# Kernel tuning notes

Hardware: AMD Instinct MI355X
Metric: run time of the kernel (lower is better)

Reference implementation:

```python
import jax, jax.numpy as jnp
import numpy as np

B, T, D, SD, CHUNK = 4, 4096, 1024, 512, 32


def setup_inputs() -> dict:
    key = jax.random.key(0)
    ks = jax.random.split(key, 6)
    sc_in = 1.0 / np.sqrt(D)
    sc_out = 1.0 / np.sqrt(2 * SD)
    return {
        "x": jax.random.normal(ks[0], (B, T, D), jnp.float32),
        "Wt": jax.random.normal(ks[1], (D, SD), jnp.float32) * sc_in,
        "bt": jnp.zeros((SD,), jnp.float32),
        "Wr": jax.random.normal(ks[2], (D, SD), jnp.float32) * sc_in,
        "br": jnp.zeros((SD,), jnp.float32),
        "Wi": jax.random.normal(ks[3], (D, 2 * SD), jnp.float32) * sc_in,
        "bi": jnp.zeros((2 * SD,), jnp.float32),
        "Wo": jax.random.normal(ks[4], (2 * SD, D), jnp.float32) * sc_out,
        "bo": jnp.zeros((D,), jnp.float32),
        "gamma": jnp.ones((D,), jnp.float32),
        "beta": jnp.zeros((D,), jnp.float32),
    }


def _rotation_scan(theta, retain, b_r, b_i, chunk):
    # theta/retain/b_*: [B, T, d]. Chunked linear recurrence h[t]=a[t]*h[t-1]+b[t]
    # with a[t] = retain[t]*e^{i theta[t]}, done in log-magnitude/angle space.
    Bsz, Tlen, d = theta.shape
    K = min(chunk, Tlen)
    n = Tlen // K  # T assumed divisible by K (4096 / 32)
    resh = lambda a: a.reshape(Bsz, n, K, d).transpose(1, 0, 2, 3)  # [n,B,K,d]
    th_c, rt_c, br_c, bi_c = resh(theta), resh(retain), resh(b_r), resh(b_i)

    def step(carry, xs):
        h_r, h_i = carry  # [B, d]
        th, rt, cb_r, cb_i = xs  # [B, K, d]
        cum_log_mag = jnp.cumsum(jnp.log(jnp.clip(rt, 1e-6, None)), axis=1)
        cum_mag = jnp.exp(cum_log_mag)
        cum_th = jnp.cumsum(th, axis=1)
        cum_cos = jnp.cos(cum_th)
        cum_sin = jnp.sin(cum_th)
        cum_a_r = cum_mag * cum_cos
        cum_a_i = cum_mag * cum_sin
        inv_mag = 1.0 / jnp.clip(cum_mag, 1e-8, None)
        inv_r = inv_mag * cum_cos          # cos(-t) = cos(t)
        inv_i = -inv_mag * cum_sin         # sin(-t) = -sin(t)
        scaled_b_r = inv_r * cb_r - inv_i * cb_i
        scaled_b_i = inv_r * cb_i + inv_i * cb_r
        cum_b_r = jnp.cumsum(scaled_b_r, axis=1)
        cum_b_i = jnp.cumsum(scaled_b_i, axis=1)
        tot_r = h_r[:, None] + cum_b_r
        tot_i = h_i[:, None] + cum_b_i
        ch_r = cum_a_r * tot_r - cum_a_i * tot_i
        ch_i = cum_a_r * tot_i + cum_a_i * tot_r
        return (ch_r[:, -1], ch_i[:, -1]), (ch_r, ch_i)

    h0 = (jnp.zeros((Bsz, d), theta.dtype), jnp.zeros((Bsz, d), theta.dtype))
    _, (out_r, out_i) = jax.lax.scan(step, h0, (th_c, rt_c, br_c, bi_c))
    back = lambda a: a.transpose(1, 0, 2, 3).reshape(Bsz, Tlen, d)
    return back(out_r), back(out_i)


def reference(x, Wt, bt, Wr, br, Wi, bi, Wo, bo, gamma, beta):
    d = Wt.shape[1]
    theta = x @ Wt + bt                       # [B,T,d]
    retain = jax.nn.sigmoid(x @ Wr + br)      # [B,T,d]
    inp = x @ Wi + bi                          # [B,T,2d]
    inp_r, inp_i = inp[..., :d], inp[..., d:]
    drive = 1.0 - retain
    out_r, out_i = _rotation_scan(theta, retain, drive * inp_r, drive * inp_i, CHUNK)
    out = jnp.concatenate([out_r, out_i], axis=-1)  # [B,T,2d]
    y = x + out @ Wo + bo
    mu = jnp.mean(y, axis=-1, keepdims=True)
    var = jnp.var(y, axis=-1, keepdims=True)
    return (y - mu) / jnp.sqrt(var + 1e-5) * gamma + beta
```

## Files before the change

kernel.cpp:

```cpp
#include <hip/hip_runtime.h>
#include <cstdint>


typedef __bf16 bf16x8 __attribute__((ext_vector_type(8)));
typedef float  f32x4  __attribute__((ext_vector_type(4)));
typedef ushort u16x8  __attribute__((ext_vector_type(8)));

#define AS1 __attribute__((address_space(1)))
#define AS3 __attribute__((address_space(3)))

__device__ __forceinline__ void gload16(const void* g, void* l) {
  __builtin_amdgcn_global_load_lds((const AS1 void*)g, (AS3 void*)l, 16, 0, 0);
}

__device__ __forceinline__ ushort f2bf(float f) {
  union { float f; uint32_t u; } v; v.f = f;
  uint32_t u = v.u;
  uint32_t r = u + 0x7FFFu + ((u >> 16) & 1u);
  return (ushort)(r >> 16);
}
__device__ __forceinline__ float bf2f(ushort u) {
  union { uint32_t x; float f; } v; v.x = (uint32_t)u << 16; return v.f;
}

__global__ __launch_bounds__(256) void tconv(const float* __restrict__ src, int R, int C,
                                             ushort* __restrict__ dst, int row_off) {
  __shared__ float tile[32][33];
  int tx = threadIdx.x, ty = threadIdx.y;
  int rb = blockIdx.y * 32, cb = blockIdx.x * 32;
#pragma unroll
  for (int yy = 0; yy < 4; ++yy) {
    int r = rb + ty + yy * 8;
    tile[ty + yy * 8][tx] = src[(size_t)r * C + cb + tx];
  }
  __syncthreads();
#pragma unroll
  for (int yy = 0; yy < 4; ++yy) {
    int c = cb + ty + yy * 8;
    dst[(size_t)(row_off + c) * R + rb + tx] = f2bf(tile[tx][ty + yy * 8]);
  }
}

__global__ __launch_bounds__(256) void pack_bias(const float* __restrict__ bt,
                                                 const float* __restrict__ br,
                                                 const float* __restrict__ bi,
                                                 float* __restrict__ bcat) {
  int i = blockIdx.x * 256 + threadIdx.x;
  bcat[i] = (i < 512) ? bt[i] : (i < 1024 ? br[i - 512] : bi[i - 1024]);
}

__global__ __launch_bounds__(256) void xconv(const float4* __restrict__ src,
                                             ushort* __restrict__ dst, int n4) {
  int i = blockIdx.x * 256 + threadIdx.x;
  if (i < n4) {
    float4 v = src[i];
    ushort4 o;
    o.x = f2bf(v.x); o.y = f2bf(v.y); o.z = f2bf(v.z); o.w = f2bf(v.w);
    *(ushort4*)(dst + (size_t)i * 4) = o;
  }
}

template <int BM>
__global__ __launch_bounds__(512, 2) void gemm256(const ushort* __restrict__ A,
                                                  const ushort* __restrict__ Bt,
                                                  ushort* __restrict__ C,
                                                  const float* __restrict__ bias,
                                                  int M, int N, int K, int nbn) {
  constexpr int MI = BM / 32;
  constexpr int II = BM / 128;
  constexpr int STAGE_USH = 2 * (BM * 64 + 256 * 64);
  constexpr int CT_USH = BM * 256;
  constexpr int SM_USH = (STAGE_USH > CT_USH) ? STAGE_USH : CT_USH;
  __shared__ alignas(16) ushort smem[SM_USH];
  ushort* const As0 = smem;
  ushort* const Bs0 = smem + 2 * BM * 64;

  const int cpx = gridDim.x >> 3;
  const int wg = ((int)blockIdx.x & 7) * cpx + ((int)blockIdx.x >> 3);
  const int bm = wg / nbn, bn = wg % nbn;

  const int t = threadIdx.x;
  const int l = t & 63, w = t >> 6;
  const int wm = w >> 2, wn = w & 3;
  const int r = l & 15, kq = l >> 4;

  const size_t a0 = (size_t)bm * BM * K;
  const size_t b0 = (size_t)bn * 256 * K;

  const int srow = t >> 3;
  const int sslot = (t & 7) ^ (srow & 7);
  const ushort* gA = A + a0 + (size_t)srow * K + sslot * 8;
  const ushort* gB = Bt + b0 + (size_t)srow * K + sslot * 8;
  const int lboff = w * 1024 + l * 16;

  f32x4 acc[MI][4] = {};
  const int NKT = K >> 6;

#define STGA(buf, kt, u) \
  gload16(gA + (size_t)((u) * 64) * K + (size_t)(kt) * 64, \
          (char*)(As0 + (buf) * BM * 64) + (u) * 8192 + lboff)
#define STGB(buf, kt, u) \
  gload16(gB + (size_t)((u) * 64) * K + (size_t)(kt) * 64, \
          (char*)(Bs0 + (buf) * 256 * 64) + (u) * 8192 + lboff)

#define QUAD(ph)                                                               \
  do {                                                                         \
    _Pragma("unroll")                                                          \
    for (int ii = 0; ii < II; ++ii) {                                          \
      bf16x8 aF[2];                                                            \
      const int rowa = wm * (BM / 2) + ((ph) * II + ii) * 16 + r;              \
      _Pragma("unroll")                                                        \
      for (int ks = 0; ks < 2; ++ks) {                                         \
        const int j = (ks * 4 + kq) ^ (r & 7);                                 \
        aF[ks] = *(const bf16x8*)&pA[rowa * 64 + j * 8];                       \
      }                                                                        \
      __builtin_amdgcn_s_setprio(1);                                           \
      _Pragma("unroll")                                                        \
      for (int jn = 0; jn < 4; ++jn)                                           \
        _Pragma("unroll")                                                      \
        for (int ks = 0; ks < 2; ++ks)                                         \
          acc[(ph) * II + ii][jn] = __builtin_amdgcn_mfma_f32_16x16x32_bf16(   \
              aF[ks], bF[jn][ks], acc[(ph) * II + ii][jn], 0, 0, 0);           \
      __builtin_amdgcn_s_setprio(0);                                           \
    }                                                                          \
  } while (0)

  STGB(0, 0, 0); STGB(0, 0, 1); STGB(0, 0, 2); STGB(0, 0, 3);
  if constexpr (BM == 256) { STGA(0, 0, 0); STGA(0, 0, 2); STGA(0, 0, 1); STGA(0, 0, 3); }
  else                     { STGA(0, 0, 0); STGA(0, 0, 1); }

  for (int kt = 0; kt < NKT; ++kt) {
    const int cur = kt & 1, nxt = cur ^ 1;
    const bool hn = (kt + 1 < NKT);
    const ushort* pA = As0 + cur * BM * 64;
    const ushort* pB = Bs0 + cur * 256 * 64;
    if (hn) { STGB(nxt, kt + 1, 0); STGB(nxt, kt + 1, 1); }
    if constexpr (BM == 256) {
      if (hn) asm volatile("s_waitcnt vmcnt(4)" ::: "memory");
      else    asm volatile("s_waitcnt vmcnt(2)" ::: "memory");
    } else {
      if (hn) asm volatile("s_waitcnt vmcnt(2)" ::: "memory");
      else    asm volatile("s_waitcnt vmcnt(0)" ::: "memory");
    }
    __builtin_amdgcn_s_barrier();
    asm volatile("" ::: "memory");
    bf16x8 bF[4][2];
#pragma unroll
    for (int jn = 0; jn < 4; ++jn) {
      const int rowb = wn * 64 + jn * 16 + r;
#pragma unroll
      for (int ks = 0; ks < 2; ++ks) {
        const int j = (ks * 4 + kq) ^ (r & 7);
        bF[jn][ks] = *(const bf16x8*)&pB[rowb * 64 + j * 8];
      }
    }
    QUAD(0);
    if (hn) { STGB(nxt, kt + 1, 2); STGB(nxt, kt + 1, 3); }
    QUAD(1);
    if (hn) {
      if constexpr (BM == 256) { STGA(nxt, kt + 1, 0); STGA(nxt, kt + 1, 2); }
      else                     { STGA(nxt, kt + 1, 0); }
    }
    if constexpr (BM == 256) {
      if (hn) asm volatile("s_waitcnt vmcnt(6)" ::: "memory");
      else    asm volatile("s_waitcnt vmcnt(0)" ::: "memory");
    }
    __builtin_amdgcn_s_barrier();
    asm volatile("" ::: "memory");
    QUAD(2);
    if (hn) {
      if constexpr (BM == 256) { STGA(nxt, kt + 1, 1); STGA(nxt, kt + 1, 3); }
      else                     { STGA(nxt, kt + 1, 1); }
    }
    QUAD(3);
  }
#undef STGA
#undef STGB
#undef QUAD

  asm volatile("s_waitcnt lgkmcnt(0) vmcnt(0)" ::: "memory");
  __builtin_amdgcn_s_barrier();

  const int q4 = (l >> 4) * 4;
  float bvj[4];
#pragma unroll
  for (int jn = 0; jn < 4; ++jn) {
    const int col = wn * 64 + jn * 16 + r;
    bvj[jn] = bias ? bias[bn * 256 + col] : 0.f;
  }
#pragma unroll
  for (int i = 0; i < MI; ++i) {
#pragma unroll
    for (int jn = 0; jn < 4; ++jn) {
      const int col = wn * 64 + jn * 16 + r;
      const int chunk = col >> 3;
#pragma unroll
      for (int q = 0; q < 4; ++q) {
        const int rowl = wm * (BM / 2) + i * 16 + q4 + q;
        const int pch = chunk ^ (rowl & 7);
        smem[rowl * 256 + pch * 8 + (col & 7)] = f2bf(acc[i][jn][q] + bvj[jn]);
      }
    }
  }
  __builtin_amdgcn_s_barrier();

  const int rrow0 = t >> 5;
  const int rch = t & 31;
#pragma unroll
  for (int p = 0; p < BM / 16; ++p) {
    const int rowl = p * 16 + rrow0;
    const int pch = rch ^ (rowl & 7);
    u16x8 vv = *(const u16x8*)&smem[rowl * 256 + pch * 8];
    const size_t grow = (size_t)(bm * BM + rowl);
    *(u16x8*)&C[grow * N + bn * 256 + rch * 8] = vv;
  }
}

__global__ __launch_bounds__(256) void scan_k1(const ushort* __restrict__ lin,
                                               float4* __restrict__ agg) {
  int bd = blockIdx.x * 256 + threadIdx.x;
  int c  = blockIdx.y;
  int b  = bd >> 9, d = bd & 511;
  const ushort* base = lin + ((size_t)b * 4096 + (size_t)c * 32) * 2048;
  float cth = 0.f, cbr = 0.f, cbi = 0.f;
  float cm = 1.f, cs = 1.f, sn = 0.f;
#pragma unroll 4
  for (int t = 0; t < 32; ++t) {
    const ushort* row = base + (size_t)t * 2048;
    float th = bf2f(row[d]);
    float z  = bf2f(row[512 + d]);
    float ir = bf2f(row[1024 + d]);
    float ii = bf2f(row[1536 + d]);
    float rt = __fdividef(1.f, 1.f + __expf(-z));
    cm *= fmaxf(rt, 1e-6f);
    cth += th;
    float s_, c_;
    __sincosf(cth, &s_, &c_);
    float im = __fdividef(1.f, fmaxf(cm, 1e-8f));
    float invr = im * c_, invi = -im * s_;
    float drive = 1.f - rt;
    float br_ = drive * ir, bi_ = drive * ii;
    cbr += invr * br_ - invi * bi_;
    cbi += invr * bi_ + invi * br_;
    cs = c_; sn = s_;
  }
  agg[(size_t)c * 2048 + bd] = make_float4(cm * cs, cm * sn, cbr, cbi);
}

__global__ __launch_bounds__(256) void scan_k2(const float4* __restrict__ agg,
                                               float2* __restrict__ h0) {
  int bd = blockIdx.x * 256 + threadIdx.x;
  float hr = 0.f, hi = 0.f;
  for (int cg = 0; cg < 16; ++cg) {
    float4 a[8];
#pragma unroll
    for (int u = 0; u < 8; ++u) a[u] = agg[(size_t)(cg * 8 + u) * 2048 + bd];
#pragma unroll
    for (int u = 0; u < 8; ++u) {
      h0[(size_t)(cg * 8 + u) * 2048 + bd] = make_float2(hr, hi);
      float tr = hr + a[u].z, ti = hi + a[u].w;
      hr = a[u].x * tr - a[u].y * ti;
      hi = a[u].x * ti + a[u].y * tr;
    }
  }
}

__global__ __launch_bounds__(256) void scan_k3(const ushort* __restrict__ lin,
                                               const float2* __restrict__ h0,
                                               ushort* __restrict__ outb) {
  int bd = blockIdx.x * 256 + threadIdx.x;
  int c  = blockIdx.y;
  int b  = bd >> 9, d = bd & 511;
  const ushort* base = lin + ((size_t)b * 4096 + (size_t)c * 32) * 2048;
  float2 h = h0[(size_t)c * 2048 + bd];
  float cth = 0.f, cbr = 0.f, cbi = 0.f, cm = 1.f;
#pragma unroll 4
  for (int t = 0; t < 32; ++t) {
    const ushort* row = base + (size_t)t * 2048;
    float th = bf2f(row[d]);
    float z  = bf2f(row[512 + d]);
    float ir = bf2f(row[1024 + d]);
    float ii = bf2f(row[1536 + d]);
    float rt = __fdividef(1.f, 1.f + __expf(-z));
    cm *= fmaxf(rt, 1e-6f);
    cth += th;
    float s_, c_;
    __sincosf(cth, &s_, &c_);
    float im = __fdividef(1.f, fmaxf(cm, 1e-8f));
    float invr = im * c_, invi = -im * s_;
    float drive = 1.f - rt;
    float br_ = drive * ir, bi_ = drive * ii;
    cbr += invr * br_ - invi * bi_;
    cbi += invr * bi_ + invi * br_;
    float ar = cm * c_, ai = cm * s_;
    float tr = h.x + cbr, ti = h.y + cbi;
    float orr = ar * tr - ai * ti;
    float oii = ar * ti + ai * tr;
    size_t rowo = ((size_t)b * 4096 + (size_t)c * 32 + t) * 1024;
    outb[rowo + d] = f2bf(orr);
    outb[rowo + 512 + d] = f2bf(oii);
  }
}

__global__ __launch_bounds__(256) void ln_k(const ushort* __restrict__ yb,
                                            const ushort* __restrict__ xb,
                                            const float* __restrict__ gamma,
                                            const float* __restrict__ beta,
                                            float* __restrict__ out) {
  int row = blockIdx.x;
  ushort4 uy = ((const ushort4*)(yb + (size_t)row * 1024))[threadIdx.x];
  ushort4 ux = ((const ushort4*)(xb + (size_t)row * 1024))[threadIdx.x];
  float4 v;
  v.x = bf2f(uy.x) + bf2f(ux.x);
  v.y = bf2f(uy.y) + bf2f(ux.y);
  v.z = bf2f(uy.z) + bf2f(ux.z);
  v.w = bf2f(uy.w) + bf2f(ux.w);
  float s  = v.x + v.y + v.z + v.w;
  float s2 = v.x * v.x + v.y * v.y + v.z * v.z + v.w * v.w;
#pragma unroll
  for (int off = 32; off > 0; off >>= 1) {
    s  += __shfl_down(s, off);
    s2 += __shfl_down(s2, off);
  }
  __shared__ float red[8];
  __shared__ float mv[2];
  int l = threadIdx.x & 63, w = threadIdx.x >> 6;
  if (l == 0) { red[w] = s; red[4 + w] = s2; }
  __syncthreads();
  if (threadIdx.x == 0) {
    float ts = red[0] + red[1] + red[2] + red[3];
    float t2 = red[4] + red[5] + red[6] + red[7];
    float mu = ts * (1.f / 1024.f);
    float var = t2 * (1.f / 1024.f) - mu * mu;
    mv[0] = mu;
    mv[1] = 1.f / sqrtf(var + 1e-5f);
  }
  __syncthreads();
  float mu = mv[0], rstd = mv[1];
  const float4* g4 = (const float4*)gamma;
  const float4* b4 = (const float4*)beta;
  float4 gv = g4[threadIdx.x], bv = b4[threadIdx.x];
  float4 o;
  o.x = (v.x - mu) * rstd * gv.x + bv.x;
  o.y = (v.y - mu) * rstd * gv.y + bv.y;
  o.z = (v.z - mu) * rstd * gv.z + bv.z;
  o.w = (v.w - mu) * rstd * gv.w + bv.w;
  ((float4*)(out + (size_t)row * 1024))[threadIdx.x] = o;
}

extern "C" void kernel_launch(void* const* d_in, const int* in_sizes, int n_in,
                              void* d_out, int out_size, void* d_ws, size_t ws_size,
                              hipStream_t stream) {
  (void)in_sizes; (void)n_in; (void)out_size; (void)ws_size;
  const float* x  = (const float*)d_in[0];
  const float* Wt = (const float*)d_in[1];
  const float* bt = (const float*)d_in[2];
  const float* Wr = (const float*)d_in[3];
  const float* br = (const float*)d_in[4];
  const float* Wi = (const float*)d_in[5];
  const float* bi = (const float*)d_in[6];
  const float* Wo = (const float*)d_in[7];
  const float* bo = (const float*)d_in[8];
  const float* gamma = (const float*)d_in[9];
  const float* beta  = (const float*)d_in[10];

  char* ws = (char*)d_ws;
  ushort* wcat_t = (ushort*)(ws);
  ushort* wo_t   = (ushort*)(ws + ((size_t)4  << 20));
  float*  bcat   = (float*) (ws + ((size_t)6  << 20));
  float4* agg    = (float4*)(ws + ((size_t)8  << 20));
  float2* h0     = (float2*)(ws + ((size_t)12 << 20));
  ushort* xb     = (ushort*)(ws + ((size_t)16 << 20));
  ushort* outb   = (ushort*)(ws + ((size_t)48 << 20));
  ushort* linb   = (ushort*)(ws + ((size_t)80 << 20));
  ushort* yb     = (ushort*)(ws + ((size_t)80 << 20));

  tconv<<<dim3(512 / 32, 1024 / 32), dim3(32, 8), 0, stream>>>(Wt, 1024, 512, wcat_t, 0);
  tconv<<<dim3(512 / 32, 1024 / 32), dim3(32, 8), 0, stream>>>(Wr, 1024, 512, wcat_t, 512);
  tconv<<<dim3(1024 / 32, 1024 / 32), dim3(32, 8), 0, stream>>>(Wi, 1024, 1024, wcat_t, 1024);
  tconv<<<dim3(1024 / 32, 1024 / 32), dim3(32, 8), 0, stream>>>(Wo, 1024, 1024, wo_t, 0);
  pack_bias<<<8, 256, 0, stream>>>(bt, br, bi, bcat);
  xconv<<<16384, 256, 0, stream>>>((const float4*)x, xb, 4194304);

  gemm256<256><<<512, 512, 0, stream>>>(xb, wcat_t, linb, bcat, 16384, 2048, 1024, 8);

  scan_k1<<<dim3(8, 128), 256, 0, stream>>>(linb, agg);
  scan_k2<<<8, 256, 0, stream>>>(agg, h0);
  scan_k3<<<dim3(8, 128), 256, 0, stream>>>(linb, h0, outb);

  gemm256<128><<<512, 512, 0, stream>>>(outb, wo_t, yb, bo, 16384, 1024, 1024, 4);

  ln_k<<<16384, 256, 0, stream>>>(yb, xb, gamma, beta, (float*)d_out);
}
```

Baseline: 213.3 us.

## Restructure GEMM mainloop into 4 barrier-separated phases with B prefetched two tiles ahead

Reorganizes the bf16 MFMA GEMM main loop into four phases, each loading its A fragments from LDS, issuing a slice of global-to-LDS staging, then running MFMAs between barriers. The B tile is now prefetched two k-steps ahead into the current buffer once it has been consumed, while A is prefetched one step ahead. The aim is to deepen the load pipeline and interleave LDS reads, global loads and MFMAs more evenly. In exchange it adds two barriers per phase (eight per k-step) and more fragment registers, and it depends on the hand-tuned vmcnt counts being correct.

Measured after the change: 217.4 us. About the same (+1.9%).

```diff
diff --git a/kernel.cpp b/kernel.cpp
--- a/kernel.cpp
+++ b/kernel.cpp
@@ -103,80 +103,98 @@
   gload16(gB + (size_t)((u) * 64) * K + (size_t)(kt) * 64, \
           (char*)(Bs0 + (buf) * 256 * 64) + (u) * 8192 + lboff)
 
-#define QUAD(ph)                                                               \
-  do {                                                                         \
+#define PHASE(ph, STAGE_STMT, WAIT_STMT)                                       \
+  {                                                                            \
+    bf16x8 aF[II][2];                                                          \
     _Pragma("unroll")                                                          \
     for (int ii = 0; ii < II; ++ii) {                                          \
-      bf16x8 aF[2];                                                            \
       const int rowa = wm * (BM / 2) + ((ph) * II + ii) * 16 + r;              \
       _Pragma("unroll")                                                        \
       for (int ks = 0; ks < 2; ++ks) {                                         \
         const int j = (ks * 4 + kq) ^ (r & 7);                                 \
-        aF[ks] = *(const bf16x8*)&pA[rowa * 64 + j * 8];                       \
+        aF[ii][ks] = *(const bf16x8*)&pA[rowa * 64 + j * 8];                   \
       }                                                                        \
-      __builtin_amdgcn_s_setprio(1);                                           \
+    }                                                                          \
+    STAGE_STMT;                                                                \
+    WAIT_STMT;                                                                 \
+    asm volatile("" ::: "memory");                                             \
+    __builtin_amdgcn_s_barrier();                                              \
+    __builtin_amdgcn_s_setprio(1);                                             \
+    _Pragma("unroll")                                                          \
+    for (int ii = 0; ii < II; ++ii)                                            \
       _Pragma("unroll")                                                        \
       for (int jn = 0; jn < 4; ++jn)                                           \
         _Pragma("unroll")                                                      \
         for (int ks = 0; ks < 2; ++ks)                                         \
           acc[(ph) * II + ii][jn] = __builtin_amdgcn_mfma_f32_16x16x32_bf16(   \
-              aF[ks], bF[jn][ks], acc[(ph) * II + ii][jn], 0, 0, 0);           \
-      __builtin_amdgcn_s_setprio(0);                                           \
-    }                                                                          \
-  } while (0)
+              aF[ii][ks], bF[jn][ks], acc[(ph) * II + ii][jn], 0, 0, 0);       \
+    __builtin_amdgcn_s_setprio(0);                                             \
+    asm volatile("" ::: "memory");                                             \
+    __builtin_amdgcn_s_barrier();                                              \
+  }
 
   STGB(0, 0, 0); STGB(0, 0, 1); STGB(0, 0, 2); STGB(0, 0, 3);
-  if constexpr (BM == 256) { STGA(0, 0, 0); STGA(0, 0, 2); STGA(0, 0, 1); STGA(0, 0, 3); }
-  else                     { STGA(0, 0, 0); STGA(0, 0, 1); }
+  STGA(0, 0, 0); STGA(0, 0, 1);
+  if constexpr (BM == 256) { STGA(0, 0, 2); STGA(0, 0, 3); }
+  STGB(1, 1, 0); STGB(1, 1, 1); STGB(1, 1, 2); STGB(1, 1, 3);
+  asm volatile("s_waitcnt vmcnt(4)" ::: "memory");
+  __builtin_amdgcn_s_barrier();
 
   for (int kt = 0; kt < NKT; ++kt) {
     const int cur = kt & 1, nxt = cur ^ 1;
-    const bool hn = (kt + 1 < NKT);
     const ushort* pA = As0 + cur * BM * 64;
     const ushort* pB = Bs0 + cur * 256 * 64;
-    if (hn) { STGB(nxt, kt + 1, 0); STGB(nxt, kt + 1, 1); }
-    if constexpr (BM == 256) {
-      if (hn) asm volatile("s_waitcnt vmcnt(4)" ::: "memory");
-      else    asm volatile("s_waitcnt vmcnt(2)" ::: "memory");
-    } else {
-      if (hn) asm volatile("s_waitcnt vmcnt(2)" ::: "memory");
-      else    asm volatile("s_waitcnt vmcnt(0)" ::: "memory");
+    bf16x8 bF[4][2];
+    {
+#pragma unroll
+      for (int jn = 0; jn < 4; ++jn) {
+        const int rowb = wn * 64 + jn * 16 + r;
+#pragma unroll
+        for (int ks = 0; ks < 2; ++ks) {
+          const int j = (ks * 4 + kq) ^ (r & 7);
+          bF[jn][ks] = *(const bf16x8*)&pB[rowb * 64 + j * 8];
+        }
+      }
+      bf16x8 aF[II][2];
+#pragma unroll
+      for (int ii = 0; ii < II; ++ii) {
+        const int rowa = wm * (BM / 2) + ii * 16 + r;
+#pragma unroll
+        for (int ks = 0; ks < 2; ++ks) {
+          const int j = (ks * 4 + kq) ^ (r & 7);
+          aF[ii][ks] = *(const bf16x8*)&pA[rowa * 64 + j * 8];
+        }
+      }
+      if (kt + 1 < NKT) {
+        STGA(nxt, kt + 1, 0); STGA(nxt, kt + 1, 1);
+        if constexpr (BM == 256) { STGA(nxt, kt + 1, 2); STGA(nxt, kt + 1, 3); }
+      }
+      asm volatile("" ::: "memory");
+      __builtin_amdgcn_s_barrier();
+      __builtin_amdgcn_s_setprio(1);
+#pragma unroll
+      for (int ii = 0; ii < II; ++ii)
+#pragma unroll
+        for (int jn = 0; jn < 4; ++jn)
+#pragma unroll
+          for (int ks = 0; ks < 2; ++ks)
+            acc[ii][jn] = __builtin_amdgcn_mfma_f32_16x16x32_bf16(
+                aF[ii][ks], bF[jn][ks], acc[ii][jn], 0, 0, 0);
+      __builtin_amdgcn_s_setprio(0);
+      asm volatile("" ::: "memory");
+      __builtin_amdgcn_s_barrier();
     }
-    __builtin_amdgcn_s_barrier();
-    asm volatile("" ::: "memory");
-    bf16x8 bF[4][2];
-#pragma unroll
-    for (int jn = 0; jn < 4; ++jn) {
-      const int rowb = wn * 64 + jn * 16 + r;
-#pragma unroll
-      for (int ks = 0; ks < 2; ++ks) {
-        const int j = (ks * 4 + kq) ^ (r & 7);
-        bF[jn][ks] = *(const bf16x8*)&pB[rowb * 64 + j * 8];
-      }
-    }
-    QUAD(0);
-    if (hn) { STGB(nxt, kt + 1, 2); STGB(nxt, kt + 1, 3); }
-    QUAD(1);
-    if (hn) {
-      if constexpr (BM == 256) { STGA(nxt, kt + 1, 0); STGA(nxt, kt + 1, 2); }
-      else                     { STGA(nxt, kt + 1, 0); }
-    }
-    if constexpr (BM == 256) {
-      if (hn) asm volatile("s_waitcnt vmcnt(6)" ::: "memory");
-      else    asm volatile("s_waitcnt vmcnt(0)" ::: "memory");
-    }
-    __builtin_amdgcn_s_barrier();
-    asm volatile("" ::: "memory");
-    QUAD(2);
-    if (hn) {
-      if constexpr (BM == 256) { STGA(nxt, kt + 1, 1); STGA(nxt, kt + 1, 3); }
-      else                     { STGA(nxt, kt + 1, 1); }
-    }
-    QUAD(3);
+    PHASE(1,
+          if (kt + 2 < NKT) { STGB(cur, kt + 2, 0); STGB(cur, kt + 2, 1); }, );
+    PHASE(2,
+          if (kt + 2 < NKT) { STGB(cur, kt + 2, 2); STGB(cur, kt + 2, 3); }, );
+    PHASE(3, ,
+          if (kt + 2 < NKT) { asm volatile("s_waitcnt vmcnt(4)" ::: "memory"); }
+          else if (kt + 1 < NKT) { asm volatile("s_waitcnt vmcnt(0)" ::: "memory"); });
   }
 #undef STGA
 #undef STGB
-#undef QUAD
+#undef PHASE
 
   asm volatile("s_waitcnt lgkmcnt(0) vmcnt(0)" ::: "memory");
   __builtin_amdgcn_s_barrier();
```
